# Kernel optimization log

Measured on AMD Instinct MI355X. Metric: run time of the kernel, lower is better.

The kernel has to match this reference:

```python
import jax, jax.numpy as jnp
import numpy as np

B, T, C = 256, 256, 147
BPM, H_DIM, NH = 32, 64, 4
HD = H_DIM // NH


def setup_inputs() -> dict:
    key = jax.random.key(0)
    ks = jax.random.split(key, 12)
    def lin(k, fan_in, fan_out):
        bound = 1.0 / np.sqrt(fan_in)
        kw, kb = jax.random.split(k)
        W = jax.random.uniform(kw, (fan_in, fan_out), jnp.float32, -bound, bound)
        b = jax.random.uniform(kb, (fan_out,), jnp.float32, -bound, bound)
        return W, b
    Wq, bq = lin(ks[0], C, H_DIM)
    Wk, bk = lin(ks[1], C, H_DIM)
    Wv, bv = lin(ks[2], C, H_DIM)
    Wb, bb = lin(ks[3], BPM, H_DIM)
    Wo, bo = lin(ks[4], H_DIM, C)
    pose = jax.random.normal(ks[5], (B, T, C), jnp.float32)
    bpm_emb = jax.random.normal(ks[6], (B, BPM), jnp.float32)
    return {"pose": pose, "bpm_emb": bpm_emb,
            "Wq": Wq, "bq": bq, "Wk": Wk, "bk": bk, "Wv": Wv, "bv": bv,
            "Wb": Wb, "bb": bb, "Wo": Wo, "bo": bo}


def reference(pose, bpm_emb, Wq, bq, Wk, bk, Wv, bv, Wb, bb, Wo, bo):
    Bb, Tt, Cc = pose.shape
    scale = HD ** -0.5
    # projections -> [B, H, T, hd]
    def split_heads(x):
        return x.reshape(Bb, Tt, NH, HD).transpose(0, 2, 1, 3)
    q = split_heads(pose @ Wq + bq)
    k = split_heads(pose @ Wk + bk)
    v = split_heads(pose @ Wv + bv)
    # bpm-conditioned key bias: [B, H, 1, hd]
    bpm_feat = (bpm_emb @ Wb + bb).reshape(Bb, 1, NH, HD).transpose(0, 2, 1, 3)
    k = k + bpm_feat
    # attention
    scores = jnp.einsum('bhqd,bhkd->bhqk', q, k) * scale
    attn = jax.nn.softmax(scores, axis=-1)
    out = jnp.einsum('bhqk,bhkd->bhqd', attn, v)
    out = out.transpose(0, 2, 1, 3).reshape(Bb, Tt, NH * HD)
    return out @ Wo + bo
```

## Files before the change

kernel.cpp:

```cpp
#include <hip/hip_runtime.h>

constexpr int kC = 147, kH = 64, kBPM = 32;

typedef __attribute__((ext_vector_type(8)))  short bf16x8;
typedef __attribute__((ext_vector_type(4)))  float f32x4;
typedef __attribute__((ext_vector_type(16))) float f32x16;
typedef __attribute__((ext_vector_type(2)))  unsigned u32x2;
typedef __attribute__((ext_vector_type(4)))  unsigned u32x4;

__device__ __forceinline__ short f2bf(float f) {
    unsigned u = __builtin_bit_cast(unsigned, f);
    u += 0x7fffu + ((u >> 16) & 1u);
    return (short)(u >> 16);
}
__device__ __forceinline__ unsigned cvt_pk(float lo, float hi) {
    unsigned r;
    asm("v_cvt_pk_bf16_f32 %0, %1, %2" : "=v"(r) : "v"(lo), "v"(hi));
    return r;
}
#define MFMA16(a,b,c) __builtin_amdgcn_mfma_f32_16x16x32_bf16((a),(b),(c),0,0,0)
#define MFMA32(a,b,c) __builtin_amdgcn_mfma_f32_32x32x16_bf16((a),(b),(c),0,0,0)

#if __has_builtin(__builtin_amdgcn_exp2f)
  #define EXP2(x) __builtin_amdgcn_exp2f(x)
#else
  #define EXP2(x) __expf((x) * 0.6931471805599453f)
#endif
constexpr float kQScale = 0.25f * 1.4426950408889634f;

constexpr int QS  = 72;
constexpr int VS  = 264;
constexpr int WSS = 168;
constexpr int WOS = 72;

__device__ __forceinline__ void stage_w_regs(const float* wr ,
                                             short* Ws, int tid) {
    #pragma unroll
    for (int it = 0; it < 5; ++it) {
        const int i = it * 1024 + tid;
        const int c = i & 63, k = (i >> 6) * 2;
        *(unsigned*)&Ws[c * WSS + (k ^ (((c >> 3) & 3) << 3))]
            = cvt_pk(wr[2*it], wr[2*it + 1]);
    }
}

__global__ __launch_bounds__(1024, 4) void fused_kernel(
    const float* __restrict__ pose, const float* __restrict__ bpm_emb,
    const float* __restrict__ Wq, const float* __restrict__ bq,
    const float* __restrict__ Wk, const float* __restrict__ bk,
    const float* __restrict__ Wv, const float* __restrict__ bv,
    const float* __restrict__ Wb, const float* __restrict__ bb,
    const float* __restrict__ Wo, const float* __restrict__ bo,
    float* __restrict__ out)
{
    __shared__ __align__(16) short qs[256 * QS];
    __shared__ __align__(16) short ks_[256 * QS];
    __shared__ __align__(16) short vt[kH * VS];
    __shared__ __align__(16) short Ws[11520];
    __shared__ float bias_s[192];

    const int tid = threadIdx.x;
    const int w = tid >> 6, lane = tid & 63;
    const int ll = lane & 15, lq = lane >> 4;
    const int lm = lane & 31, lh = lane >> 5;
    const int b = blockIdx.x;
    const size_t pbase = (size_t)b * 256 * kC;

    float wq_r[10], wk_r[10], wv_r[10], wo_r[10];
    #pragma unroll
    for (int it = 0; it < 5; ++it) {
        const int i = it * 1024 + tid;
        const int c = i & 63, k = (i >> 6) * 2;
        const bool b0 = k < kC, b1 = k + 1 < kC;
        wq_r[2*it]   = b0 ? Wq[k * kH + c] * kQScale : 0.f;
        wq_r[2*it+1] = b1 ? Wq[(k + 1) * kH + c] * kQScale : 0.f;
        wk_r[2*it]   = b0 ? Wk[k * kH + c] : 0.f;
        wk_r[2*it+1] = b1 ? Wk[(k + 1) * kH + c] : 0.f;
        wv_r[2*it]   = b0 ? Wv[k * kH + c] : 0.f;
        wv_r[2*it+1] = b1 ? Wv[(k + 1) * kH + c] : 0.f;
        const int n = i % 160, ko = (i / 160) * 2;
        wo_r[2*it]   = (n < kC) ? Wo[ko * kC + n] : 0.f;
        wo_r[2*it+1] = (n < kC) ? Wo[(ko + 1) * kC + n] : 0.f;
    }

    bf16x8 pf[5];
    {
        const int row = w * 16 + ll;
        const float* prow = pose + pbase + (size_t)row * kC;
        #pragma unroll
        for (int ksp = 0; ksp < 5; ++ksp) {
            const int c0 = ksp * 32 + lq * 8;
            float v[8];
            if (c0 + 8 <= kC) {
                const float4 f0 = *(const float4*)(prow + c0);
                const float4 f1 = *(const float4*)(prow + c0 + 4);
                v[0]=f0.x; v[1]=f0.y; v[2]=f0.z; v[3]=f0.w;
                v[4]=f1.x; v[5]=f1.y; v[6]=f1.z; v[7]=f1.w;
            } else {
                #pragma unroll
                for (int e = 0; e < 8; ++e) v[e] = (c0 + e < kC) ? prow[c0 + e] : 0.f;
            }
            const u32x4 t = { cvt_pk(v[0], v[1]), cvt_pk(v[2], v[3]),
                              cvt_pk(v[4], v[5]), cvt_pk(v[6], v[7]) };
            pf[ksp] = __builtin_bit_cast(bf16x8, t);
        }
    }
    if (tid < 192) {
        const int m = tid >> 6, c = tid & 63;
        float a = ((m == 0) ? bq : (m == 1) ? bk : bv)[c];
        if (m == 1) {
            a += bb[c];
            #pragma unroll
            for (int k2 = 0; k2 < kBPM; ++k2)
                a = fmaf(bpm_emb[b * kBPM + k2], Wb[k2 * kH + c], a);
        }
        if (m == 0) a *= kQScale;
        bias_s[tid] = a;
    }
    stage_w_regs(wq_r, Ws, tid);
    __syncthreads();

    #pragma unroll
    for (int m = 0; m < 3; ++m) {
        f32x4 acc[4];
        #pragma unroll
        for (int mt = 0; mt < 4; ++mt) acc[mt] = (f32x4){0.f,0.f,0.f,0.f};
        #pragma unroll
        for (int ksp = 0; ksp < 5; ++ksp)
            #pragma unroll
            for (int mt = 0; mt < 4; ++mt) {
                const int c = mt * 16 + ll;
                const int key = ((c >> 3) & 3) << 3;
                const bf16x8 wf = *(const bf16x8*)(Ws + c * WSS + ((ksp*32 + lq*8) ^ key));
                acc[mt] = MFMA16(wf, pf[ksp], acc[mt]);
            }
        __syncthreads();
        if (m == 0)      stage_w_regs(wk_r, Ws, tid);
        else if (m == 1) stage_w_regs(wv_r, Ws, tid);
        else {
            #pragma unroll
            for (int it = 0; it < 5; ++it) {
                const int i = it * 1024 + tid;
                const int n = i % 160, k = (i / 160) * 2;
                *(unsigned*)&Ws[n * WOS + (k ^ (((n >> 3) & 3) << 3))]
                    = cvt_pk(wo_r[2*it], wo_r[2*it + 1]);
            }
        }
        const int row = w * 16 + ll;
        #pragma unroll
        for (int mt = 0; mt < 4; ++mt) {
            const int c0 = mt * 16 + 4 * lq;
            const float4 bv4 = *(const float4*)&bias_s[m * kH + c0];
            if (m < 2) {
                const u32x2 pk = { cvt_pk(acc[mt][0] + bv4.x, acc[mt][1] + bv4.y),
                                   cvt_pk(acc[mt][2] + bv4.z, acc[mt][3] + bv4.w) };
                *(u32x2*)((m == 0 ? qs : ks_) + row * QS + c0) = pk;
            } else {
                vt[(c0 + 0) * VS + row] = f2bf(acc[mt][0] + bv4.x);
                vt[(c0 + 1) * VS + row] = f2bf(acc[mt][1] + bv4.y);
                vt[(c0 + 2) * VS + row] = f2bf(acc[mt][2] + bv4.z);
                vt[(c0 + 3) * VS + row] = f2bf(acc[mt][3] + bv4.w);
            }
        }
        __syncthreads();
    }

    const int h = w & 3;
    const int q0 = (w >> 2) * 64;
    bf16x8 qf[2];
    #pragma unroll
    for (int s32 = 0; s32 < 2; ++s32)
        qf[s32] = *(const bf16x8*)(qs + (q0 + s32*32 + lm) * QS + h*16 + lh*8);

    f32x16 oacc[2];
    #pragma unroll
    for (int s32 = 0; s32 < 2; ++s32)
        oacc[s32] = (f32x16){0.f,0.f,0.f,0.f,0.f,0.f,0.f,0.f,
                             0.f,0.f,0.f,0.f,0.f,0.f,0.f,0.f};
    float lp[2] = {0.f, 0.f};
    const int vrow = h * 16 + (lm & 15);
    const f32x16 z16 = {0.f,0.f,0.f,0.f,0.f,0.f,0.f,0.f,
                        0.f,0.f,0.f,0.f,0.f,0.f,0.f,0.f};

    #pragma unroll 2
    for (int jb = 0; jb < 8; ++jb) {
        const int j0 = jb * 32;
        const bf16x8 kf  = *(const bf16x8*)(ks_ + (j0 + lm) * QS + h*16 + lh*8);
        const bf16x8 va0 = *(const bf16x8*)(vt + vrow * VS + j0 + lh*8);
        const bf16x8 va1 = *(const bf16x8*)(vt + vrow * VS + j0 + 16 + lh*8);
        #pragma unroll
        for (int s32 = 0; s32 < 2; ++s32) {
            const f32x16 s = MFMA32(kf, qf[s32], z16);
            float sum = 0.f;
            unsigned u[8];
            #pragma unroll
            for (int g = 0; g < 4; ++g) {
                const float p0 = EXP2(s[4*g + 0]);
                const float p1 = EXP2(s[4*g + 1]);
                const float p2 = EXP2(s[4*g + 2]);
                const float p3 = EXP2(s[4*g + 3]);
                sum += (p0 + p1) + (p2 + p3);
                u[2*g]   = cvt_pk(p0, p1);
                u[2*g+1] = cvt_pk(p2, p3);
            }
            lp[s32] += sum;
            unsigned a0 = u[0], a1 = u[1], b0 = u[2], b1 = u[3];
            asm("v_permlane32_swap_b32 %0, %1" : "+v"(a0), "+v"(b0));
            asm("v_permlane32_swap_b32 %0, %1" : "+v"(a1), "+v"(b1));
            unsigned c0 = u[4], c1 = u[5], d0 = u[6], d1 = u[7];
            asm("v_permlane32_swap_b32 %0, %1" : "+v"(c0), "+v"(d0));
            asm("v_permlane32_swap_b32 %0, %1" : "+v"(c1), "+v"(d1));
            const u32x4 pb0 = { a0, a1, b0, b1 };
            const u32x4 pb1 = { c0, c1, d0, d1 };
            oacc[s32] = MFMA32(va0, __builtin_bit_cast(bf16x8, pb0), oacc[s32]);
            oacc[s32] = MFMA32(va1, __builtin_bit_cast(bf16x8, pb1), oacc[s32]);
        }
    }
    #pragma unroll
    for (int s32 = 0; s32 < 2; ++s32) {
        const float l2 = lp[s32] + __shfl_xor(lp[s32], 32);
        const float inv = 1.f / l2;
        const int row = q0 + s32 * 32 + lm;
        const u32x2 pkA = { cvt_pk(oacc[s32][0] * inv, oacc[s32][1] * inv),
                            cvt_pk(oacc[s32][2] * inv, oacc[s32][3] * inv) };
        *(u32x2*)(qs + row * QS + h*16 + 4*lh) = pkA;
        const u32x2 pkB = { cvt_pk(oacc[s32][4] * inv, oacc[s32][5] * inv),
                            cvt_pk(oacc[s32][6] * inv, oacc[s32][7] * inv) };
        *(u32x2*)(qs + row * QS + h*16 + 8 + 4*lh) = pkB;
    }
    __syncthreads();

    bf16x8 xf[2];
    #pragma unroll
    for (int k2 = 0; k2 < 2; ++k2)
        xf[k2] = *(const bf16x8*)(qs + (w*16 + ll) * QS + k2*32 + lq*8);

    f32x4 po[10];
    #pragma unroll
    for (int mt = 0; mt < 10; ++mt) po[mt] = (f32x4){0.f,0.f,0.f,0.f};
    #pragma unroll
    for (int k2 = 0; k2 < 2; ++k2)
        #pragma unroll
        for (int mt = 0; mt < 10; ++mt) {
            const int n = mt * 16 + ll;
            const int key = ((n >> 3) & 3) << 3;
            const bf16x8 wf = *(const bf16x8*)(Ws + n * WOS + ((k2*32 + lq*8) ^ key));
            po[mt] = MFMA16(wf, xf[k2], po[mt]);
        }
    {
        const int row = w * 16 + ll;
        float* orow = out + ((size_t)b * 256 + row) * kC;
        #pragma unroll
        for (int mt = 0; mt < 10; ++mt) {
            const int c0 = mt * 16 + 4 * lq;
            if (mt < 9) {
                const float4 bv4 = *(const float4*)(bo + c0);
                float4 o;
                o.x = po[mt][0] + bv4.x; o.y = po[mt][1] + bv4.y;
                o.z = po[mt][2] + bv4.z; o.w = po[mt][3] + bv4.w;
                *(float4*)(orow + c0) = o;
            } else {
                #pragma unroll
                for (int r = 0; r < 4; ++r) {
                    const int c = c0 + r;
                    if (c < kC) orow[c] = po[mt][r] + bo[c];
                }
            }
        }
    }
}

extern "C" void kernel_launch(void* const* d_in, const int* in_sizes, int n_in,
                              void* d_out, int out_size, void* d_ws, size_t ws_size,
                              hipStream_t stream) {
    const float* pose    = (const float*)d_in[0];
    const float* bpm_emb = (const float*)d_in[1];
    const float* Wq = (const float*)d_in[2];  const float* bq = (const float*)d_in[3];
    const float* Wk = (const float*)d_in[4];  const float* bk = (const float*)d_in[5];
    const float* Wv = (const float*)d_in[6];  const float* bv = (const float*)d_in[7];
    const float* Wb = (const float*)d_in[8];  const float* bb = (const float*)d_in[9];
    const float* Wo = (const float*)d_in[10]; const float* bo = (const float*)d_in[11];
    float* out = (float*)d_out;

    fused_kernel<<<256, 1024, 0, stream>>>(
        pose, bpm_emb, Wq, bq, Wk, bk, Wv, bv, Wb, bb, Wo, bo, out);
}
```

Measured before the change: 132.0 us.

## Tile projection GEMMs as 32x32 warp blocks and double-buffer weight staging

Each wave now computes a 32-row by 32-column (or 80-column for the output projection) tile, so each weight fragment read from LDS feeds two MFMAs instead of one, halving weight LDS traffic. The weight staging buffer is split into two (WsA/WsB), which removes the barrier between computing with one projection's weights and writing the next one's. The cost is more LDS (an extra ~23KB), which may reduce occupancy, plus more accumulator and fragment registers per wave.

Result: slower. 139.5 us (+5.7%).

```diff
diff --git a/kernel.cpp b/kernel.cpp
--- a/kernel.cpp
+++ b/kernel.cpp
@@ -56,7 +56,8 @@
     __shared__ __align__(16) short qs[256 * QS];
     __shared__ __align__(16) short ks_[256 * QS];
     __shared__ __align__(16) short vt[kH * VS];
-    __shared__ __align__(16) short Ws[11520];
+    __shared__ __align__(16) short WsA[11520];
+    __shared__ __align__(16) short WsB[11520];
     __shared__ float bias_s[192];
 
     const int tid = threadIdx.x;
@@ -83,9 +84,11 @@
         wo_r[2*it+1] = (n < kC) ? Wo[(ko + 1) * kC + n] : 0.f;
     }
 
-    bf16x8 pf[5];
-    {
-        const int row = w * 16 + ll;
+    const int wr = w & 7, wc = w >> 3;
+    bf16x8 pf[2][5];
+    #pragma unroll
+    for (int rt = 0; rt < 2; ++rt) {
+        const int row = wr * 32 + rt * 16 + ll;
         const float* prow = pose + pbase + (size_t)row * kC;
         #pragma unroll
         for (int ksp = 0; ksp < 5; ++ksp) {
@@ -102,7 +105,7 @@
             }
             const u32x4 t = { cvt_pk(v[0], v[1]), cvt_pk(v[2], v[3]),
                               cvt_pk(v[4], v[5]), cvt_pk(v[6], v[7]) };
-            pf[ksp] = __builtin_bit_cast(bf16x8, t);
+            pf[rt][ksp] = __builtin_bit_cast(bf16x8, t);
         }
     }
     if (tid < 192) {
@@ -117,49 +120,56 @@
         if (m == 0) a *= kQScale;
         bias_s[tid] = a;
     }
-    stage_w_regs(wq_r, Ws, tid);
+    stage_w_regs(wq_r, WsA, tid);
     __syncthreads();
 
     #pragma unroll
     for (int m = 0; m < 3; ++m) {
-        f32x4 acc[4];
-        #pragma unroll
-        for (int mt = 0; mt < 4; ++mt) acc[mt] = (f32x4){0.f,0.f,0.f,0.f};
+        const short* R = (m == 1) ? WsB : WsA;
+        f32x4 acc[2][2];
+        #pragma unroll
+        for (int rt = 0; rt < 2; ++rt)
+            #pragma unroll
+            for (int mt = 0; mt < 2; ++mt) acc[rt][mt] = (f32x4){0.f,0.f,0.f,0.f};
         #pragma unroll
         for (int ksp = 0; ksp < 5; ++ksp)
             #pragma unroll
-            for (int mt = 0; mt < 4; ++mt) {
-                const int c = mt * 16 + ll;
+            for (int mt = 0; mt < 2; ++mt) {
+                const int c = wc * 32 + mt * 16 + ll;
                 const int key = ((c >> 3) & 3) << 3;
-                const bf16x8 wf = *(const bf16x8*)(Ws + c * WSS + ((ksp*32 + lq*8) ^ key));
-                acc[mt] = MFMA16(wf, pf[ksp], acc[mt]);
-            }
-        __syncthreads();
-        if (m == 0)      stage_w_regs(wk_r, Ws, tid);
-        else if (m == 1) stage_w_regs(wv_r, Ws, tid);
+                const bf16x8 wf = *(const bf16x8*)(R + c * WSS + ((ksp*32 + lq*8) ^ key));
+                #pragma unroll
+                for (int rt = 0; rt < 2; ++rt)
+                    acc[rt][mt] = MFMA16(wf, pf[rt][ksp], acc[rt][mt]);
+            }
+        if (m == 0)      stage_w_regs(wk_r, WsB, tid);
+        else if (m == 1) stage_w_regs(wv_r, WsA, tid);
         else {
             #pragma unroll
             for (int it = 0; it < 5; ++it) {
                 const int i = it * 1024 + tid;
                 const int n = i % 160, k = (i / 160) * 2;
-                *(unsigned*)&Ws[n * WOS + (k ^ (((n >> 3) & 3) << 3))]
+                *(unsigned*)&WsB[n * WOS + (k ^ (((n >> 3) & 3) << 3))]
                     = cvt_pk(wo_r[2*it], wo_r[2*it + 1]);
             }
         }
-        const int row = w * 16 + ll;
-        #pragma unroll
-        for (int mt = 0; mt < 4; ++mt) {
-            const int c0 = mt * 16 + 4 * lq;
-            const float4 bv4 = *(const float4*)&bias_s[m * kH + c0];
-            if (m < 2) {
-                const u32x2 pk = { cvt_pk(acc[mt][0] + bv4.x, acc[mt][1] + bv4.y),
-                                   cvt_pk(acc[mt][2] + bv4.z, acc[mt][3] + bv4.w) };
-                *(u32x2*)((m == 0 ? qs : ks_) + row * QS + c0) = pk;
-            } else {
-                vt[(c0 + 0) * VS + row] = f2bf(acc[mt][0] + bv4.x);
-                vt[(c0 + 1) * VS + row] = f2bf(acc[mt][1] + bv4.y);
-                vt[(c0 + 2) * VS + row] = f2bf(acc[mt][2] + bv4.z);
-                vt[(c0 + 3) * VS + row] = f2bf(acc[mt][3] + bv4.w);
+        #pragma unroll
+        for (int rt = 0; rt < 2; ++rt) {
+            const int row = wr * 32 + rt * 16 + ll;
+            #pragma unroll
+            for (int mt = 0; mt < 2; ++mt) {
+                const int c0 = wc * 32 + mt * 16 + 4 * lq;
+                const float4 bv4 = *(const float4*)&bias_s[m * kH + c0];
+                if (m < 2) {
+                    const u32x2 pk = { cvt_pk(acc[rt][mt][0] + bv4.x, acc[rt][mt][1] + bv4.y),
+                                       cvt_pk(acc[rt][mt][2] + bv4.z, acc[rt][mt][3] + bv4.w) };
+                    *(u32x2*)((m == 0 ? qs : ks_) + row * QS + c0) = pk;
+                } else {
+                    vt[(c0 + 0) * VS + row] = f2bf(acc[rt][mt][0] + bv4.x);
+                    vt[(c0 + 1) * VS + row] = f2bf(acc[rt][mt][1] + bv4.y);
+                    vt[(c0 + 2) * VS + row] = f2bf(acc[rt][mt][2] + bv4.z);
+                    vt[(c0 + 3) * VS + row] = f2bf(acc[rt][mt][3] + bv4.w);
+                }
             }
         }
         __syncthreads();
@@ -230,40 +240,47 @@
     }
     __syncthreads();
 
-    bf16x8 xf[2];
+    bf16x8 xf[2][2];
+    #pragma unroll
+    for (int rt = 0; rt < 2; ++rt)
+        #pragma unroll
+        for (int k2 = 0; k2 < 2; ++k2)
+            xf[rt][k2] = *(const bf16x8*)(qs + (wr*32 + rt*16 + ll) * QS + k2*32 + lq*8);
+
+    f32x4 po[2][5];
+    #pragma unroll
+    for (int rt = 0; rt < 2; ++rt)
+        #pragma unroll
+        for (int mt = 0; mt < 5; ++mt) po[rt][mt] = (f32x4){0.f,0.f,0.f,0.f};
     #pragma unroll
     for (int k2 = 0; k2 < 2; ++k2)
-        xf[k2] = *(const bf16x8*)(qs + (w*16 + ll) * QS + k2*32 + lq*8);
-
-    f32x4 po[10];
-    #pragma unroll
-    for (int mt = 0; mt < 10; ++mt) po[mt] = (f32x4){0.f,0.f,0.f,0.f};
-    #pragma unroll
-    for (int k2 = 0; k2 < 2; ++k2)
-        #pragma unroll
-        for (int mt = 0; mt < 10; ++mt) {
-            const int n = mt * 16 + ll;
+        #pragma unroll
+        for (int mt = 0; mt < 5; ++mt) {
+            const int n = wc * 80 + mt * 16 + ll;
             const int key = ((n >> 3) & 3) << 3;
-            const bf16x8 wf = *(const bf16x8*)(Ws + n * WOS + ((k2*32 + lq*8) ^ key));
-            po[mt] = MFMA16(wf, xf[k2], po[mt]);
-        }
-    {
-        const int row = w * 16 + ll;
+            const bf16x8 wf = *(const bf16x8*)(WsB + n * WOS + ((k2*32 + lq*8) ^ key));
+            #pragma unroll
+            for (int rt = 0; rt < 2; ++rt)
+                po[rt][mt] = MFMA16(wf, xf[rt][k2], po[rt][mt]);
+        }
+    #pragma unroll
+    for (int rt = 0; rt < 2; ++rt) {
+        const int row = wr * 32 + rt * 16 + ll;
         float* orow = out + ((size_t)b * 256 + row) * kC;
         #pragma unroll
-        for (int mt = 0; mt < 10; ++mt) {
-            const int c0 = mt * 16 + 4 * lq;
-            if (mt < 9) {
+        for (int mt = 0; mt < 5; ++mt) {
+            const int c0 = wc * 80 + mt * 16 + 4 * lq;
+            if (wc == 0 || mt < 4) {
                 const float4 bv4 = *(const float4*)(bo + c0);
                 float4 o;
-                o.x = po[mt][0] + bv4.x; o.y = po[mt][1] + bv4.y;
-                o.z = po[mt][2] + bv4.z; o.w = po[mt][3] + bv4.w;
+                o.x = po[rt][mt][0] + bv4.x; o.y = po[rt][mt][1] + bv4.y;
+                o.z = po[rt][mt][2] + bv4.z; o.w = po[rt][mt][3] + bv4.w;
                 *(float4*)(orow + c0) = o;
             } else {
                 #pragma unroll
                 for (int r = 0; r < 4; ++r) {
                     const int c = c0 + r;
-                    if (c < kC) orow[c] = po[mt][r] + bo[c];
+                    if (c < kC) orow[c] = po[rt][mt][r] + bo[c];
                 }
             }
         }
```

## Double-buffer projection weights in LDS and defer per-stage weight loads

Applied to the files above, without the earlier changes.

Splits the single LDS weight buffer into two, so the next projection's weights (K, V, then Wo) are staged into the other buffer while the current projection's MFMAs read from the first. This removes one barrier per stage. The global loads of Wk, Wv and Wo now happen just before they are needed instead of all at kernel start, which lowers live register pressure and overlaps those loads with compute. In exchange the kernel uses about 23 KB more LDS per block, and the launch-bounds hint is restated as waves_per_eu(4,4).

Result: no change. 130.0 us (-1.5%).

```diff
diff --git a/kernel.cpp b/kernel.cpp
--- a/kernel.cpp
+++ b/kernel.cpp
@@ -44,7 +44,25 @@
     }
 }
 
-__global__ __launch_bounds__(1024, 4) void fused_kernel(
+#define QKV_MFMA(Rbuf)                                                        \
+    {                                                                         \
+        _Pragma("unroll")                                                     \
+        for (int mt = 0; mt < 4; ++mt) acc[mt] = (f32x4){0.f,0.f,0.f,0.f};    \
+        _Pragma("unroll")                                                     \
+        for (int ksp = 0; ksp < 5; ++ksp)                                     \
+            _Pragma("unroll")                                                 \
+            for (int mt = 0; mt < 4; ++mt) {                                  \
+                const int c = mt * 16 + ll;                                   \
+                const int key = ((c >> 3) & 3) << 3;                          \
+                const bf16x8 wf = *(const bf16x8*)((Rbuf) + c * WSS +         \
+                                      ((ksp * 32 + lq * 8) ^ key));           \
+                acc[mt] = MFMA16(wf, pf[ksp], acc[mt]);                       \
+            }                                                                 \
+    }
+
+__global__ __launch_bounds__(1024)
+__attribute__((amdgpu_waves_per_eu(4, 4)))
+void fused_kernel(
     const float* __restrict__ pose, const float* __restrict__ bpm_emb,
     const float* __restrict__ Wq, const float* __restrict__ bq,
     const float* __restrict__ Wk, const float* __restrict__ bk,
@@ -56,7 +74,8 @@
     __shared__ __align__(16) short qs[256 * QS];
     __shared__ __align__(16) short ks_[256 * QS];
     __shared__ __align__(16) short vt[kH * VS];
-    __shared__ __align__(16) short Ws[11520];
+    __shared__ __align__(16) short WsA[11520];
+    __shared__ __align__(16) short WsB[11520];
     __shared__ float bias_s[192];
 
     const int tid = threadIdx.x;
@@ -65,23 +84,6 @@
     const int lm = lane & 31, lh = lane >> 5;
     const int b = blockIdx.x;
     const size_t pbase = (size_t)b * 256 * kC;
-
-    float wq_r[10], wk_r[10], wv_r[10], wo_r[10];
-    #pragma unroll
-    for (int it = 0; it < 5; ++it) {
-        const int i = it * 1024 + tid;
-        const int c = i & 63, k = (i >> 6) * 2;
-        const bool b0 = k < kC, b1 = k + 1 < kC;
-        wq_r[2*it]   = b0 ? Wq[k * kH + c] * kQScale : 0.f;
-        wq_r[2*it+1] = b1 ? Wq[(k + 1) * kH + c] * kQScale : 0.f;
-        wk_r[2*it]   = b0 ? Wk[k * kH + c] : 0.f;
-        wk_r[2*it+1] = b1 ? Wk[(k + 1) * kH + c] : 0.f;
-        wv_r[2*it]   = b0 ? Wv[k * kH + c] : 0.f;
-        wv_r[2*it+1] = b1 ? Wv[(k + 1) * kH + c] : 0.f;
-        const int n = i % 160, ko = (i / 160) * 2;
-        wo_r[2*it]   = (n < kC) ? Wo[ko * kC + n] : 0.f;
-        wo_r[2*it+1] = (n < kC) ? Wo[(ko + 1) * kC + n] : 0.f;
-    }
 
     bf16x8 pf[5];
     {
@@ -105,6 +107,14 @@
             pf[ksp] = __builtin_bit_cast(bf16x8, t);
         }
     }
+    float wq_r[10];
+    #pragma unroll
+    for (int it = 0; it < 5; ++it) {
+        const int i = it * 1024 + tid;
+        const int c = i & 63, k = (i >> 6) * 2;
+        wq_r[2*it]   = (k     < kC) ? Wq[k * kH + c] * kQScale : 0.f;
+        wq_r[2*it+1] = (k + 1 < kC) ? Wq[(k + 1) * kH + c] * kQScale : 0.f;
+    }
     if (tid < 192) {
         const int m = tid >> 6, c = tid & 63;
         float a = ((m == 0) ? bq : (m == 1) ? bk : bv)[c];
@@ -117,49 +127,91 @@
         if (m == 0) a *= kQScale;
         bias_s[tid] = a;
     }
-    stage_w_regs(wq_r, Ws, tid);
+    stage_w_regs(wq_r, WsA, tid);
     __syncthreads();
 
-    #pragma unroll
-    for (int m = 0; m < 3; ++m) {
+    {
+        float wk_r[10];
+        #pragma unroll
+        for (int it = 0; it < 5; ++it) {
+            const int i = it * 1024 + tid;
+            const int c = i & 63, k = (i >> 6) * 2;
+            wk_r[2*it]   = (k     < kC) ? Wk[k * kH + c] : 0.f;
+            wk_r[2*it+1] = (k + 1 < kC) ? Wk[(k + 1) * kH + c] : 0.f;
+        }
         f32x4 acc[4];
-        #pragma unroll
-        for (int mt = 0; mt < 4; ++mt) acc[mt] = (f32x4){0.f,0.f,0.f,0.f};
-        #pragma unroll
-        for (int ksp = 0; ksp < 5; ++ksp)
+        QKV_MFMA(WsA);
+        stage_w_regs(wk_r, WsB, tid);
+        float wv_r[10];
+        #pragma unroll
+        for (int it = 0; it < 5; ++it) {
+            const int i = it * 1024 + tid;
+            const int c = i & 63, k = (i >> 6) * 2;
+            wv_r[2*it]   = (k     < kC) ? Wv[k * kH + c] : 0.f;
+            wv_r[2*it+1] = (k + 1 < kC) ? Wv[(k + 1) * kH + c] : 0.f;
+        }
+        {
+            const int row = w * 16 + ll;
             #pragma unroll
             for (int mt = 0; mt < 4; ++mt) {
-                const int c = mt * 16 + ll;
-                const int key = ((c >> 3) & 3) << 3;
-                const bf16x8 wf = *(const bf16x8*)(Ws + c * WSS + ((ksp*32 + lq*8) ^ key));
-                acc[mt] = MFMA16(wf, pf[ksp], acc[mt]);
-            }
-        __syncthreads();
-        if (m == 0)      stage_w_regs(wk_r, Ws, tid);
-        else if (m == 1) stage_w_regs(wv_r, Ws, tid);
-        else {
-            #pragma unroll
-            for (int it = 0; it < 5; ++it) {
-                const int i = it * 1024 + tid;
-                const int n = i % 160, k = (i / 160) * 2;
-                *(unsigned*)&Ws[n * WOS + (k ^ (((n >> 3) & 3) << 3))]
-                    = cvt_pk(wo_r[2*it], wo_r[2*it + 1]);
-            }
-        }
-        const int row = w * 16 + ll;
-        #pragma unroll
-        for (int mt = 0; mt < 4; ++mt) {
-            const int c0 = mt * 16 + 4 * lq;
-            const float4 bv4 = *(const float4*)&bias_s[m * kH + c0];
-            if (m < 2) {
+                const int c0 = mt * 16 + 4 * lq;
+                const float4 bv4 = *(const float4*)&bias_s[0 * kH + c0];
                 const u32x2 pk = { cvt_pk(acc[mt][0] + bv4.x, acc[mt][1] + bv4.y),
                                    cvt_pk(acc[mt][2] + bv4.z, acc[mt][3] + bv4.w) };
-                *(u32x2*)((m == 0 ? qs : ks_) + row * QS + c0) = pk;
-            } else {
-                vt[(c0 + 0) * VS + row] = f2bf(acc[mt][0] + bv4.x);
-                vt[(c0 + 1) * VS + row] = f2bf(acc[mt][1] + bv4.y);
-                vt[(c0 + 2) * VS + row] = f2bf(acc[mt][2] + bv4.z);
-                vt[(c0 + 3) * VS + row] = f2bf(acc[mt][3] + bv4.w);
+                *(u32x2*)(qs + row * QS + c0) = pk;
+            }
+        }
+        __syncthreads();
+
+        f32x4 acc1[4];
+        {
+            f32x4* acc = acc1;
+            QKV_MFMA(WsB);
+        }
+        stage_w_regs(wv_r, WsA, tid);
+        float wo_r[10];
+        #pragma unroll
+        for (int it = 0; it < 5; ++it) {
+            const int i = it * 1024 + tid;
+            const int n = i % 160, k = (i / 160) * 2;
+            wo_r[2*it]   = (n < kC) ? Wo[k * kC + n] : 0.f;
+            wo_r[2*it+1] = (n < kC) ? Wo[(k + 1) * kC + n] : 0.f;
+        }
+        {
+            const int row = w * 16 + ll;
+            #pragma unroll
+            for (int mt = 0; mt < 4; ++mt) {
+                const int c0 = mt * 16 + 4 * lq;
+                const float4 bv4 = *(const float4*)&bias_s[1 * kH + c0];
+                const u32x2 pk = { cvt_pk(acc1[mt][0] + bv4.x, acc1[mt][1] + bv4.y),
+                                   cvt_pk(acc1[mt][2] + bv4.z, acc1[mt][3] + bv4.w) };
+                *(u32x2*)(ks_ + row * QS + c0) = pk;
+            }
+        }
+        __syncthreads();
+
+        f32x4 acc2[4];
+        {
+            f32x4* acc = acc2;
+            QKV_MFMA(WsA);
+        }
+        #pragma unroll
+        for (int it = 0; it < 5; ++it) {
+            const int i = it * 1024 + tid;
+            const int n = i % 160, k = (i / 160) * 2;
+            *(unsigned*)&WsB[n * WOS + (k ^ (((n >> 3) & 3) << 3))]
+                = cvt_pk(wo_r[2*it], wo_r[2*it + 1]);
+        }
+        {
+            const int row = w * 16 + ll;
+            #pragma unroll
+            for (int mt = 0; mt < 4; ++mt) {
+                const int c0 = mt * 16 + 4 * lq;
+                const float4 bv4 = *(const float4*)&bias_s[2 * kH + c0];
+                vt[(c0 + 0) * VS + row] = f2bf(acc2[mt][0] + bv4.x);
+                vt[(c0 + 1) * VS + row] = f2bf(acc2[mt][1] + bv4.y);
+                vt[(c0 + 2) * VS + row] = f2bf(acc2[mt][2] + bv4.z);
+                vt[(c0 + 3) * VS + row] = f2bf(acc2[mt][3] + bv4.w);
             }
         }
         __syncthreads();
@@ -244,7 +296,7 @@
         for (int mt = 0; mt < 10; ++mt) {
             const int n = mt * 16 + ll;
             const int key = ((n >> 3) & 3) << 3;
-            const bf16x8 wf = *(const bf16x8*)(Ws + n * WOS + ((k2*32 + lq*8) ^ key));
+            const bf16x8 wf = *(const bf16x8*)(WsB + n * WOS + ((k2*32 + lq*8) ^ key));
             po[mt] = MFMA16(wf, xf[k2], po[mt]);
         }
     {
```

## Split each batch across two blocks and pre-convert weights in a prep kernel

Applied to the files above, without the earlier changes.

Adds a prep kernel that converts Wq/Wk/Wv/Wo to padded bf16 layouts in workspace and precomputes the per-batch key bias. The main kernel now runs 512 blocks of 512 threads, each handling half the queries of a batch. It reads weight fragments directly from global memory instead of staging them in LDS, and uses XOR-swizzled LDS layouts without padding. This raises block-level parallelism and drops per-block weight conversion, but each block recomputes K and V for the whole sequence and adds a second launch.

After: 227.1 us. +72.1%, slower.

```diff
diff --git a/kernel.cpp b/kernel.cpp
--- a/kernel.cpp
+++ b/kernel.cpp
@@ -28,169 +28,165 @@
 #endif
 constexpr float kQScale = 0.25f * 1.4426950408889634f;
 
-constexpr int QS  = 72;
-constexpr int VS  = 264;
-constexpr int WSS = 168;
-constexpr int WOS = 72;
-
-__device__ __forceinline__ void stage_w_regs(const float* wr ,
-                                             short* Ws, int tid) {
-    #pragma unroll
-    for (int it = 0; it < 5; ++it) {
-        const int i = it * 1024 + tid;
-        const int c = i & 63, k = (i >> 6) * 2;
-        *(unsigned*)&Ws[c * WSS + (k ^ (((c >> 3) & 3) << 3))]
-            = cvt_pk(wr[2*it], wr[2*it + 1]);
-    }
-}
-
-__global__ __launch_bounds__(1024, 4) void fused_kernel(
-    const float* __restrict__ pose, const float* __restrict__ bpm_emb,
-    const float* __restrict__ Wq, const float* __restrict__ bq,
-    const float* __restrict__ Wk, const float* __restrict__ bk,
-    const float* __restrict__ Wv, const float* __restrict__ bv,
-    const float* __restrict__ Wb, const float* __restrict__ bb,
-    const float* __restrict__ Wo, const float* __restrict__ bo,
-    float* __restrict__ out)
+__global__ __launch_bounds__(128) void prep_kernel(
+    const float* __restrict__ bpm_emb,
+    const float* __restrict__ Wq, const float* __restrict__ Wk,
+    const float* __restrict__ Wv, const float* __restrict__ Wb,
+    const float* __restrict__ bk, const float* __restrict__ bb,
+    const float* __restrict__ Wo,
+    short* __restrict__ wt, float* __restrict__ kbc)
 {
-    __shared__ __align__(16) short qs[256 * QS];
-    __shared__ __align__(16) short ks_[256 * QS];
-    __shared__ __align__(16) short vt[kH * VS];
-    __shared__ __align__(16) short Ws[11520];
-    __shared__ float bias_s[192];
+    const int bid = blockIdx.x, tid = threadIdx.x;
+    if (bid < 256) {
+        if (tid < kH) {
+            const int c = tid;
+            float a = bk[c];
+            a += bb[c];
+            #pragma unroll
+            for (int j = 0; j < kBPM; ++j)
+                a = fmaf(bpm_emb[bid * kBPM + j], Wb[j * kH + c], a);
+            kbc[bid * kH + c] = a;
+        }
+    } else if (bid < 259) {
+        const int m = bid - 256;
+        const float* W = (m == 0) ? Wq : (m == 1) ? Wk : Wv;
+        const float scale = (m == 0) ? kQScale : 1.f;
+        short* dst = wt + m * 10240;
+        for (int idx = tid; idx < 64 * 160; idx += 128) {
+            const int c = idx / 160, k = idx - c * 160;
+            dst[idx] = f2bf((k < kC) ? W[k * kH + c] * scale : 0.f);
+        }
+    } else {
+        short* dst = wt + 3 * 10240;
+        for (int idx = tid; idx < 160 * 64; idx += 128) {
+            const int n = idx >> 6, k = idx & 63;
+            dst[idx] = f2bf((n < kC) ? Wo[k * kC + n] : 0.f);
+        }
+    }
+}
+
+__global__ __launch_bounds__(512, 4) void fused_kernel(
+    const float* __restrict__ pose,
+    const float* __restrict__ bq, const float* __restrict__ bv,
+    const short* __restrict__ wt, const float* __restrict__ kbc,
+    const float* __restrict__ bo, float* __restrict__ out)
+{
+    __shared__ __align__(16) short qs[128 * 64];
+    __shared__ __align__(16) short ks_[256 * 64];
+    __shared__ __align__(16) short vt[64 * 256];
 
     const int tid = threadIdx.x;
     const int w = tid >> 6, lane = tid & 63;
     const int ll = lane & 15, lq = lane >> 4;
     const int lm = lane & 31, lh = lane >> 5;
-    const int b = blockIdx.x;
+    const int b = blockIdx.x >> 1, half = blockIdx.x & 1;
     const size_t pbase = (size_t)b * 256 * kC;
-
-    float wq_r[10], wk_r[10], wv_r[10], wo_r[10];
-    #pragma unroll
-    for (int it = 0; it < 5; ++it) {
-        const int i = it * 1024 + tid;
-        const int c = i & 63, k = (i >> 6) * 2;
-        const bool b0 = k < kC, b1 = k + 1 < kC;
-        wq_r[2*it]   = b0 ? Wq[k * kH + c] * kQScale : 0.f;
-        wq_r[2*it+1] = b1 ? Wq[(k + 1) * kH + c] * kQScale : 0.f;
-        wk_r[2*it]   = b0 ? Wk[k * kH + c] : 0.f;
-        wk_r[2*it+1] = b1 ? Wk[(k + 1) * kH + c] : 0.f;
-        wv_r[2*it]   = b0 ? Wv[k * kH + c] : 0.f;
-        wv_r[2*it+1] = b1 ? Wv[(k + 1) * kH + c] : 0.f;
-        const int n = i % 160, ko = (i / 160) * 2;
-        wo_r[2*it]   = (n < kC) ? Wo[ko * kC + n] : 0.f;
-        wo_r[2*it+1] = (n < kC) ? Wo[(ko + 1) * kC + n] : 0.f;
-    }
-
-    bf16x8 pf[5];
-    {
-        const int row = w * 16 + ll;
-        const float* prow = pose + pbase + (size_t)row * kC;
-        #pragma unroll
-        for (int ksp = 0; ksp < 5; ++ksp) {
-            const int c0 = ksp * 32 + lq * 8;
-            float v[8];
-            if (c0 + 8 <= kC) {
-                const float4 f0 = *(const float4*)(prow + c0);
-                const float4 f1 = *(const float4*)(prow + c0 + 4);
-                v[0]=f0.x; v[1]=f0.y; v[2]=f0.z; v[3]=f0.w;
-                v[4]=f1.x; v[5]=f1.y; v[6]=f1.z; v[7]=f1.w;
-            } else {
+    const short* wtq = wt;
+    const short* wtk = wt + 10240;
+    const short* wtv = wt + 20480;
+    const short* wto = wt + 30720;
+
+    #pragma unroll
+    for (int pass = 0; pass < 3; ++pass) {
+        const int row = (pass < 2 ? pass * 128 : half * 128) + w * 16 + ll;
+        bf16x8 pf[5];
+        {
+            const float* prow = pose + pbase + (size_t)row * kC;
+            #pragma unroll
+            for (int ksp = 0; ksp < 5; ++ksp) {
+                const int c0 = ksp * 32 + lq * 8;
+                float v[8];
+                if (c0 + 8 <= kC) {
+                    const float4 f0 = *(const float4*)(prow + c0);
+                    const float4 f1 = *(const float4*)(prow + c0 + 4);
+                    v[0]=f0.x; v[1]=f0.y; v[2]=f0.z; v[3]=f0.w;
+                    v[4]=f1.x; v[5]=f1.y; v[6]=f1.z; v[7]=f1.w;
+                } else {
+                    #pragma unroll
+                    for (int e = 0; e < 8; ++e) v[e] = (c0 + e < kC) ? prow[c0 + e] : 0.f;
+                }
+                const u32x4 t = { cvt_pk(v[0], v[1]), cvt_pk(v[2], v[3]),
+                                  cvt_pk(v[4], v[5]), cvt_pk(v[6], v[7]) };
+                pf[ksp] = __builtin_bit_cast(bf16x8, t);
+            }
+        }
+        if (pass < 2) {
+            f32x4 accK[4], accV[4];
+            #pragma unroll
+            for (int mt = 0; mt < 4; ++mt) {
+                accK[mt] = (f32x4){0.f,0.f,0.f,0.f};
+                accV[mt] = (f32x4){0.f,0.f,0.f,0.f};
+            }
+            #pragma unroll
+            for (int ksp = 0; ksp < 5; ++ksp)
                 #pragma unroll
-                for (int e = 0; e < 8; ++e) v[e] = (c0 + e < kC) ? prow[c0 + e] : 0.f;
-            }
-            const u32x4 t = { cvt_pk(v[0], v[1]), cvt_pk(v[2], v[3]),
-                              cvt_pk(v[4], v[5]), cvt_pk(v[6], v[7]) };
-            pf[ksp] = __builtin_bit_cast(bf16x8, t);
-        }
-    }
-    if (tid < 192) {
-        const int m = tid >> 6, c = tid & 63;
-        float a = ((m == 0) ? bq : (m == 1) ? bk : bv)[c];
-        if (m == 1) {
-            a += bb[c];
-            #pragma unroll
-            for (int k2 = 0; k2 < kBPM; ++k2)
-                a = fmaf(bpm_emb[b * kBPM + k2], Wb[k2 * kH + c], a);
-        }
-        if (m == 0) a *= kQScale;
-        bias_s[tid] = a;
-    }
-    stage_w_regs(wq_r, Ws, tid);
+                for (int mt = 0; mt < 4; ++mt) {
+                    const int off = (mt * 16 + ll) * 160 + ksp * 32 + lq * 8;
+                    accK[mt] = MFMA16(*(const bf16x8*)(wtk + off), pf[ksp], accK[mt]);
+                    accV[mt] = MFMA16(*(const bf16x8*)(wtv + off), pf[ksp], accV[mt]);
+                }
+            const int rkey = (row & 7) << 3;
+            #pragma unroll
+            for (int mt = 0; mt < 4; ++mt) {
+                const int c0 = mt * 16 + 4 * lq;
+                const float4 kb4 = *(const float4*)(kbc + b * kH + c0);
+                const u32x2 pk = { cvt_pk(accK[mt][0] + kb4.x, accK[mt][1] + kb4.y),
+                                   cvt_pk(accK[mt][2] + kb4.z, accK[mt][3] + kb4.w) };
+                *(u32x2*)(ks_ + row * 64 + (c0 ^ rkey)) = pk;
+                const float4 bv4 = *(const float4*)(bv + c0);
+                vt[(c0 + 0) * 256 + (row ^ (((c0 + 0) & 7) << 3))] = f2bf(accV[mt][0] + bv4.x);
+                vt[(c0 + 1) * 256 + (row ^ (((c0 + 1) & 7) << 3))] = f2bf(accV[mt][1] + bv4.y);
+                vt[(c0 + 2) * 256 + (row ^ (((c0 + 2) & 7) << 3))] = f2bf(accV[mt][2] + bv4.z);
+                vt[(c0 + 3) * 256 + (row ^ (((c0 + 3) & 7) << 3))] = f2bf(accV[mt][3] + bv4.w);
+            }
+        } else {
+            f32x4 acc[4];
+            #pragma unroll
+            for (int mt = 0; mt < 4; ++mt) acc[mt] = (f32x4){0.f,0.f,0.f,0.f};
+            #pragma unroll
+            for (int ksp = 0; ksp < 5; ++ksp)
+                #pragma unroll
+                for (int mt = 0; mt < 4; ++mt) {
+                    const int off = (mt * 16 + ll) * 160 + ksp * 32 + lq * 8;
+                    acc[mt] = MFMA16(*(const bf16x8*)(wtq + off), pf[ksp], acc[mt]);
+                }
+            const int rl = w * 16 + ll;
+            const int rkey = (rl & 7) << 3;
+            #pragma unroll
+            for (int mt = 0; mt < 4; ++mt) {
+                const int c0 = mt * 16 + 4 * lq;
+                const float4 bq4 = *(const float4*)(bq + c0);
+                const float q0b = bq4.x * kQScale, q1b = bq4.y * kQScale;
+                const float q2b = bq4.z * kQScale, q3b = bq4.w * kQScale;
+                const u32x2 pk = { cvt_pk(acc[mt][0] + q0b, acc[mt][1] + q1b),
+                                   cvt_pk(acc[mt][2] + q2b, acc[mt][3] + q3b) };
+                *(u32x2*)(qs + rl * 64 + (c0 ^ rkey)) = pk;
+            }
+        }
+    }
     __syncthreads();
-
-    #pragma unroll
-    for (int m = 0; m < 3; ++m) {
-        f32x4 acc[4];
-        #pragma unroll
-        for (int mt = 0; mt < 4; ++mt) acc[mt] = (f32x4){0.f,0.f,0.f,0.f};
-        #pragma unroll
-        for (int ksp = 0; ksp < 5; ++ksp)
-            #pragma unroll
-            for (int mt = 0; mt < 4; ++mt) {
-                const int c = mt * 16 + ll;
-                const int key = ((c >> 3) & 3) << 3;
-                const bf16x8 wf = *(const bf16x8*)(Ws + c * WSS + ((ksp*32 + lq*8) ^ key));
-                acc[mt] = MFMA16(wf, pf[ksp], acc[mt]);
-            }
-        __syncthreads();
-        if (m == 0)      stage_w_regs(wk_r, Ws, tid);
-        else if (m == 1) stage_w_regs(wv_r, Ws, tid);
-        else {
-            #pragma unroll
-            for (int it = 0; it < 5; ++it) {
-                const int i = it * 1024 + tid;
-                const int n = i % 160, k = (i / 160) * 2;
-                *(unsigned*)&Ws[n * WOS + (k ^ (((n >> 3) & 3) << 3))]
-                    = cvt_pk(wo_r[2*it], wo_r[2*it + 1]);
-            }
-        }
-        const int row = w * 16 + ll;
-        #pragma unroll
-        for (int mt = 0; mt < 4; ++mt) {
-            const int c0 = mt * 16 + 4 * lq;
-            const float4 bv4 = *(const float4*)&bias_s[m * kH + c0];
-            if (m < 2) {
-                const u32x2 pk = { cvt_pk(acc[mt][0] + bv4.x, acc[mt][1] + bv4.y),
-                                   cvt_pk(acc[mt][2] + bv4.z, acc[mt][3] + bv4.w) };
-                *(u32x2*)((m == 0 ? qs : ks_) + row * QS + c0) = pk;
-            } else {
-                vt[(c0 + 0) * VS + row] = f2bf(acc[mt][0] + bv4.x);
-                vt[(c0 + 1) * VS + row] = f2bf(acc[mt][1] + bv4.y);
-                vt[(c0 + 2) * VS + row] = f2bf(acc[mt][2] + bv4.z);
-                vt[(c0 + 3) * VS + row] = f2bf(acc[mt][3] + bv4.w);
-            }
-        }
-        __syncthreads();
-    }
 
     const int h = w & 3;
     const int q0 = (w >> 2) * 64;
-    bf16x8 qf[2];
-    #pragma unroll
-    for (int s32 = 0; s32 < 2; ++s32)
-        qf[s32] = *(const bf16x8*)(qs + (q0 + s32*32 + lm) * QS + h*16 + lh*8);
-
-    f32x16 oacc[2];
-    #pragma unroll
-    for (int s32 = 0; s32 < 2; ++s32)
-        oacc[s32] = (f32x16){0.f,0.f,0.f,0.f,0.f,0.f,0.f,0.f,
-                             0.f,0.f,0.f,0.f,0.f,0.f,0.f,0.f};
-    float lp[2] = {0.f, 0.f};
     const int vrow = h * 16 + (lm & 15);
+    const int vkey = (vrow & 7) << 3;
+    const int ckey = (lm & 7) << 3;
     const f32x16 z16 = {0.f,0.f,0.f,0.f,0.f,0.f,0.f,0.f,
                         0.f,0.f,0.f,0.f,0.f,0.f,0.f,0.f};
 
-    #pragma unroll 2
-    for (int jb = 0; jb < 8; ++jb) {
-        const int j0 = jb * 32;
-        const bf16x8 kf  = *(const bf16x8*)(ks_ + (j0 + lm) * QS + h*16 + lh*8);
-        const bf16x8 va0 = *(const bf16x8*)(vt + vrow * VS + j0 + lh*8);
-        const bf16x8 va1 = *(const bf16x8*)(vt + vrow * VS + j0 + 16 + lh*8);
-        #pragma unroll
-        for (int s32 = 0; s32 < 2; ++s32) {
-            const f32x16 s = MFMA32(kf, qf[s32], z16);
+    #pragma unroll
+    for (int s32 = 0; s32 < 2; ++s32) {
+        const int qrow = q0 + s32 * 32 + lm;
+        const bf16x8 qf = *(const bf16x8*)(qs + qrow * 64 + ((h*16 + lh*8) ^ ckey));
+        f32x16 oacc = z16;
+        float lp = 0.f;
+        #pragma unroll 2
+        for (int jb = 0; jb < 8; ++jb) {
+            const int j0 = jb * 32;
+            const bf16x8 kf  = *(const bf16x8*)(ks_ + (j0 + lm) * 64 + ((h*16 + lh*8) ^ ckey));
+            const bf16x8 va0 = *(const bf16x8*)(vt + vrow * 256 + ((j0 + lh*8) ^ vkey));
+            const bf16x8 va1 = *(const bf16x8*)(vt + vrow * 256 + ((j0 + 16 + lh*8) ^ vkey));
+            const f32x16 s = MFMA32(kf, qf, z16);
             float sum = 0.f;
             unsigned u[8];
             #pragma unroll
@@ -203,7 +199,7 @@
                 u[2*g]   = cvt_pk(p0, p1);
                 u[2*g+1] = cvt_pk(p2, p3);
             }
-            lp[s32] += sum;
+            lp += sum;
             unsigned a0 = u[0], a1 = u[1], b0 = u[2], b1 = u[3];
             asm("v_permlane32_swap_b32 %0, %1" : "+v"(a0), "+v"(b0));
             asm("v_permlane32_swap_b32 %0, %1" : "+v"(a1), "+v"(b1));
@@ -212,58 +208,55 @@
             asm("v_permlane32_swap_b32 %0, %1" : "+v"(c1), "+v"(d1));
             const u32x4 pb0 = { a0, a1, b0, b1 };
             const u32x4 pb1 = { c0, c1, d0, d1 };
-            oacc[s32] = MFMA32(va0, __builtin_bit_cast(bf16x8, pb0), oacc[s32]);
-            oacc[s32] = MFMA32(va1, __builtin_bit_cast(bf16x8, pb1), oacc[s32]);
-        }
-    }
-    #pragma unroll
-    for (int s32 = 0; s32 < 2; ++s32) {
-        const float l2 = lp[s32] + __shfl_xor(lp[s32], 32);
+            oacc = MFMA32(va0, __builtin_bit_cast(bf16x8, pb0), oacc);
+            oacc = MFMA32(va1, __builtin_bit_cast(bf16x8, pb1), oacc);
+        }
+        const float l2 = lp + __shfl_xor(lp, 32);
         const float inv = 1.f / l2;
-        const int row = q0 + s32 * 32 + lm;
-        const u32x2 pkA = { cvt_pk(oacc[s32][0] * inv, oacc[s32][1] * inv),
-                            cvt_pk(oacc[s32][2] * inv, oacc[s32][3] * inv) };
-        *(u32x2*)(qs + row * QS + h*16 + 4*lh) = pkA;
-        const u32x2 pkB = { cvt_pk(oacc[s32][4] * inv, oacc[s32][5] * inv),
-                            cvt_pk(oacc[s32][6] * inv, oacc[s32][7] * inv) };
-        *(u32x2*)(qs + row * QS + h*16 + 8 + 4*lh) = pkB;
+        const u32x2 pkA = { cvt_pk(oacc[0] * inv, oacc[1] * inv),
+                            cvt_pk(oacc[2] * inv, oacc[3] * inv) };
+        *(u32x2*)(qs + qrow * 64 + ((h*16 + 4*lh) ^ ckey)) = pkA;
+        const u32x2 pkB = { cvt_pk(oacc[4] * inv, oacc[5] * inv),
+                            cvt_pk(oacc[6] * inv, oacc[7] * inv) };
+        *(u32x2*)(qs + qrow * 64 + ((h*16 + 8 + 4*lh) ^ ckey)) = pkB;
     }
     __syncthreads();
 
+    const int xr = w * 16 + ll;
+    const int xkey = (ll & 7) << 3;
     bf16x8 xf[2];
     #pragma unroll
     for (int k2 = 0; k2 < 2; ++k2)
-        xf[k2] = *(const bf16x8*)(qs + (w*16 + ll) * QS + k2*32 + lq*8);
-
-    f32x4 po[10];
-    #pragma unroll
-    for (int mt = 0; mt < 10; ++mt) po[mt] = (f32x4){0.f,0.f,0.f,0.f};
-    #pragma unroll
-    for (int k2 = 0; k2 < 2; ++k2)
+        xf[k2] = *(const bf16x8*)(qs + xr * 64 + ((k2*32 + lq*8) ^ xkey));
+    float* orow = out + ((size_t)b * 256 + half * 128 + xr) * kC;
+    #pragma unroll
+    for (int hmt = 0; hmt < 2; ++hmt) {
+        f32x4 po[5];
         #pragma unroll
-        for (int mt = 0; mt < 10; ++mt) {
-            const int n = mt * 16 + ll;
-            const int key = ((n >> 3) & 3) << 3;
-            const bf16x8 wf = *(const bf16x8*)(Ws + n * WOS + ((k2*32 + lq*8) ^ key));
-            po[mt] = MFMA16(wf, xf[k2], po[mt]);
-        }
-    {
-        const int row = w * 16 + ll;
-        float* orow = out + ((size_t)b * 256 + row) * kC;
+        for (int m5 = 0; m5 < 5; ++m5) po[m5] = (f32x4){0.f,0.f,0.f,0.f};
         #pragma unroll
-        for (int mt = 0; mt < 10; ++mt) {
+        for (int k2 = 0; k2 < 2; ++k2)
+            #pragma unroll
+            for (int m5 = 0; m5 < 5; ++m5) {
+                const int n = hmt * 80 + m5 * 16 + ll;
+                po[m5] = MFMA16(*(const bf16x8*)(wto + n * 64 + k2*32 + lq*8),
+                                xf[k2], po[m5]);
+            }
+        #pragma unroll
+        for (int m5 = 0; m5 < 5; ++m5) {
+            const int mt = hmt * 5 + m5;
             const int c0 = mt * 16 + 4 * lq;
             if (mt < 9) {
                 const float4 bv4 = *(const float4*)(bo + c0);
                 float4 o;
-                o.x = po[mt][0] + bv4.x; o.y = po[mt][1] + bv4.y;
-                o.z = po[mt][2] + bv4.z; o.w = po[mt][3] + bv4.w;
+                o.x = po[m5][0] + bv4.x; o.y = po[m5][1] + bv4.y;
+                o.z = po[m5][2] + bv4.z; o.w = po[m5][3] + bv4.w;
                 *(float4*)(orow + c0) = o;
             } else {
                 #pragma unroll
                 for (int r = 0; r < 4; ++r) {
                     const int c = c0 + r;
-                    if (c < kC) orow[c] = po[mt][r] + bo[c];
+                    if (c < kC) orow[c] = po[m5][r] + bo[c];
                 }
             }
         }
@@ -282,6 +275,10 @@
     const float* Wo = (const float*)d_in[10]; const float* bo = (const float*)d_in[11];
     float* out = (float*)d_out;
 
-    fused_kernel<<<256, 1024, 0, stream>>>(
-        pose, bpm_emb, Wq, bq, Wk, bk, Wv, bv, Wb, bb, Wo, bo, out);
-}
+    short* wt  = (short*)d_ws;
+    float* kbc = (float*)((char*)d_ws + 81920);
+
+    prep_kernel<<<260, 128, 0, stream>>>(bpm_emb, Wq, Wk, Wv, Wb, bk, bb, Wo,
+                                         wt, kbc);
+    fused_kernel<<<512, 512, 0, stream>>>(pose, bq, bv, wt, kbc, bo, out);
+}
```
